# Kernel tuning notes

Measured on AMD Instinct MI355X. Metric: run time of the kernel, lower is better.

Reference implementation:

```python
import jax, jax.numpy as jnp
import numpy as np

N_EMBD = 1024
N_HEAD = 16

def setup_inputs() -> dict:
    key = jax.random.key(0)
    k1, k2, k3, k4, k5 = jax.random.split(key, 5)
    C = N_EMBD
    s = 1.0 / np.sqrt(C)
    return {
        "x": jax.random.normal(k1, (2, 2048, C), dtype=jnp.float32),
        "W_attn": jax.random.normal(k2, (C, 3 * C), dtype=jnp.float32) * s,
        "b_attn": jax.random.normal(k3, (3 * C,), dtype=jnp.float32) * 0.02,
        "W_proj": jax.random.normal(k4, (C, C), dtype=jnp.float32) * s,
        "b_proj": jax.random.normal(k5, (C,), dtype=jnp.float32) * 0.02,
    }

def reference(x, W_attn, b_attn, W_proj, b_proj):
    B, T, C = x.shape
    nh = N_HEAD
    hs = C // nh
    qkv = x @ W_attn + b_attn                      # [B, T, 3C]
    q, k, v = jnp.split(qkv, 3, axis=-1)
    # [B, T, C] -> [B, nh, T, hs]
    def to_heads(t):
        return t.reshape(B, T, nh, hs).transpose(0, 2, 1, 3)
    q, k, v = to_heads(q), to_heads(k), to_heads(v)
    scale = 1.0 / np.sqrt(hs).astype(np.float32)
    att = jnp.einsum('bhqd,bhkd->bhqk', q, k) * scale   # [B, nh, T, T]
    causal = jnp.tril(jnp.ones((T, T), dtype=bool))
    att = jnp.where(causal, att, -jnp.inf)
    att = jax.nn.softmax(att, axis=-1)
    y = jnp.einsum('bhqk,bhkd->bhqd', att, v)           # [B, nh, T, hs]
    y = y.transpose(0, 2, 1, 3).reshape(B, T, C)
    return y @ W_proj + b_proj
```

## Files before the change

### kernel.cpp

```cpp
#include <hip/hip_runtime.h>
#include <hip/hip_bf16.h>
#include <math.h>

#define N_EMBD 1024
#define N_HEAD 16
#define HS 64
#define BT 4096
#define TSEQ 2048

typedef float f32x4 __attribute__((ext_vector_type(4)));
typedef short bf16x8 __attribute__((ext_vector_type(8)));
typedef unsigned short u16;

static __device__ __forceinline__ u16 f2bf(float f) {
  union { float f; unsigned int u; } c; c.f = f;
  unsigned int r = c.u + 0x7FFFu + ((c.u >> 16) & 1u);
  return (u16)(r >> 16);
}

static __device__ __forceinline__ u16 f2bf_fast(float f) {
  union { __hip_bfloat16 h; u16 u; } cv;
  cv.h = __float2bfloat16(f);
  return cv.u;
}

__global__ __launch_bounds__(256) void cvt_bf16(const float* __restrict__ in,
                                                u16* __restrict__ out, int n4) {
  int i = blockIdx.x * 256 + threadIdx.x;
  if (i < n4) {
    float4 v = ((const float4*)in)[i];
    ushort4 o;
    o.x = f2bf(v.x); o.y = f2bf(v.y); o.z = f2bf(v.z); o.w = f2bf(v.w);
    ((ushort4*)out)[i] = o;
  }
}

__global__ __launch_bounds__(256) void transpose_cvt(const float* __restrict__ W,
                                                     u16* __restrict__ Wt,
                                                     int K, int N) {
  __shared__ u16 Ls[32][36];
  const int n0 = blockIdx.x * 32, k0 = blockIdx.y * 32;
  const int t = threadIdx.x;
  {
    int kk = t >> 3, nn4 = (t & 7) * 4;
    float4 v = *(const float4*)(W + (size_t)(k0 + kk) * N + n0 + nn4);
    Ls[kk][nn4 + 0] = f2bf(v.x); Ls[kk][nn4 + 1] = f2bf(v.y);
    Ls[kk][nn4 + 2] = f2bf(v.z); Ls[kk][nn4 + 3] = f2bf(v.w);
  }
  __syncthreads();
  {
    int nn = t >> 3, kk4 = (t & 7) * 4;
    ushort4 o;
    o.x = Ls[kk4 + 0][nn]; o.y = Ls[kk4 + 1][nn];
    o.z = Ls[kk4 + 2][nn]; o.w = Ls[kk4 + 3][nn];
    *(ushort4*)(Wt + (size_t)(n0 + nn) * K + k0 + kk4) = o;
  }
}

#define BKS 32

__device__ __forceinline__ int swz(int row, int c) {
  return row * 4 + (c ^ ((row >> 1) & 3));
}

__device__ __forceinline__ void stage128x32(const u16* __restrict__ G, int ldk,
                                            u16* lds, int w, int lane) {
#pragma unroll
  for (int i = 0; i < 2; ++i) {
    int s = i * 256 + w * 64 + lane;
    int row = s >> 2, c = s & 3;
    int csrc = c ^ ((row >> 1) & 3);
    const u16* src = G + (size_t)row * ldk + csrc * 8;
    u16* dst = lds + (size_t)(i * 256 + w * 64) * 8;
    __builtin_amdgcn_global_load_lds(
        (const __attribute__((address_space(1))) void*)src,
        (__attribute__((address_space(3))) void*)dst, 16, 0, 0);
  }
}

#define GEMM_MAIN_LOOP(Aptr, Bptr, Kdim)                                        \
  __shared__ u16 sm[2][2][128 * BKS];                                           \
  const int tid = threadIdx.x, lane = tid & 63, w = tid >> 6;                   \
  const int wr = w >> 1, wc = w & 1, lrow = lane & 15, lhi = lane >> 4;         \
  const int bm = blockIdx.y * 128, bn = blockIdx.x * 128;                       \
  f32x4 acc[4][4];                                                              \
  _Pragma("unroll") for (int i = 0; i < 4; ++i)                                 \
      _Pragma("unroll") for (int j = 0; j < 4; ++j)                             \
          acc[i][j] = (f32x4){0.f, 0.f, 0.f, 0.f};                              \
  stage128x32(Aptr + (size_t)bm * Kdim, Kdim, sm[0][0], w, lane);               \
  stage128x32(Bptr + (size_t)bn * Kdim, Kdim, sm[0][1], w, lane);               \
  __syncthreads();                                                              \
  const int NT = Kdim / BKS;                                                    \
  for (int t = 0; t < NT; ++t) {                                                \
    int cur = t & 1, nxt = cur ^ 1;                                             \
    if (t + 1 < NT) {                                                           \
      stage128x32(Aptr + (size_t)bm * Kdim + (t + 1) * BKS, Kdim, sm[nxt][0],   \
                  w, lane);                                                     \
      stage128x32(Bptr + (size_t)bn * Kdim + (t + 1) * BKS, Kdim, sm[nxt][1],   \
                  w, lane);                                                     \
    }                                                                           \
    const u16* As = sm[cur][0];                                                 \
    const u16* Bs = sm[cur][1];                                                 \
    bf16x8 af[4], bfr[4];                                                       \
    _Pragma("unroll") for (int mi = 0; mi < 4; ++mi) {                          \
      int row = wr * 64 + mi * 16 + lrow;                                       \
      af[mi] = *(const bf16x8*)(As + (size_t)swz(row, lhi) * 8);                \
    }                                                                           \
    _Pragma("unroll") for (int nj = 0; nj < 4; ++nj) {                          \
      int row = wc * 64 + nj * 16 + lrow;                                       \
      bfr[nj] = *(const bf16x8*)(Bs + (size_t)swz(row, lhi) * 8);               \
    }                                                                           \
    _Pragma("unroll") for (int mi = 0; mi < 4; ++mi)                            \
        _Pragma("unroll") for (int nj = 0; nj < 4; ++nj)                        \
            acc[mi][nj] = __builtin_amdgcn_mfma_f32_16x16x32_bf16(              \
                af[mi], bfr[nj], acc[mi][nj], 0, 0, 0);                         \
    __syncthreads();                                                            \
  }

__global__ __launch_bounds__(256) void gemm_qkv_bf16(
    const u16* __restrict__ Ab, const u16* __restrict__ Btr,
    const float* __restrict__ bias,
    u16* __restrict__ Qb, u16* __restrict__ Kb, u16* __restrict__ Vt) {
  GEMM_MAIN_LOOP(Ab, Btr, N_EMBD)
  const int sector = bn >> 10;
  const float QSC = 0.125f * 1.44269504f;
#pragma unroll
  for (int nj = 0; nj < 4; ++nj) {
    int n = bn + wc * 64 + nj * 16 + lrow;
    int h = (n & 1023) >> 6, d = n & 63;
    float bv = bias[n];
#pragma unroll
    for (int mi = 0; mi < 4; ++mi) {
      int mbase = bm + wr * 64 + mi * 16 + lhi * 4;
      int bb_ = mbase >> 11, tt = mbase & 2047;
      if (sector == 0) {
#pragma unroll
        for (int r = 0; r < 4; ++r)
          Qb[((size_t)(bb_ * 16 + h) * TSEQ + tt + r) * HS + d] =
              f2bf((acc[mi][nj][r] + bv) * QSC);
      } else if (sector == 1) {
#pragma unroll
        for (int r = 0; r < 4; ++r)
          Kb[((size_t)(bb_ * 16 + h) * TSEQ + tt + r) * HS + d] =
              f2bf(acc[mi][nj][r] + bv);
      } else {
        ushort4 o;
        o.x = f2bf(acc[mi][nj][0] + bv); o.y = f2bf(acc[mi][nj][1] + bv);
        o.z = f2bf(acc[mi][nj][2] + bv); o.w = f2bf(acc[mi][nj][3] + bv);
        *(ushort4*)(Vt + ((size_t)(bb_ * 16 + h) * HS + d) * TSEQ + tt) = o;
      }
    }
  }
}

__global__ __launch_bounds__(256) void gemm_proj_bf16(
    const u16* __restrict__ Ab, const u16* __restrict__ Btr,
    const float* __restrict__ bias, float* __restrict__ C) {
  GEMM_MAIN_LOOP(Ab, Btr, N_EMBD)
#pragma unroll
  for (int nj = 0; nj < 4; ++nj) {
    int n = bn + wc * 64 + nj * 16 + lrow;
    float bv = bias[n];
#pragma unroll
    for (int mi = 0; mi < 4; ++mi) {
      int mbase = bm + wr * 64 + mi * 16 + lhi * 4;
#pragma unroll
      for (int r = 0; r < 4; ++r)
        C[(size_t)(mbase + r) * N_EMBD + n] = acc[mi][nj][r] + bv;
    }
  }
}

__device__ __forceinline__ void stage_kv(const u16* __restrict__ Kh,
                                         const u16* __restrict__ Vh,
                                         int kb, u16* kbuf, u16* vbuf,
                                         int tid, int w) {
#pragma unroll
  for (int i = 0; i < 2; ++i) {
    int s = i * 256 + tid;
    int r = s >> 3, c = s & 7;
    int cs = c ^ (r & 7);
    const u16* ksrc = Kh + (size_t)(kb + r) * HS + cs * 8;
    u16* kdst = kbuf + (size_t)(i * 256 + (w << 6)) * 8;
    __builtin_amdgcn_global_load_lds(
        (const __attribute__((address_space(1))) void*)ksrc,
        (__attribute__((address_space(3))) void*)kdst, 16, 0, 0);
    const u16* vsrc = Vh + (size_t)r * TSEQ + kb + cs * 8;
    u16* vdst = vbuf + (size_t)(i * 256 + (w << 6)) * 8;
    __builtin_amdgcn_global_load_lds(
        (const __attribute__((address_space(1))) void*)vsrc,
        (__attribute__((address_space(3))) void*)vdst, 16, 0, 0);
  }
}

__global__ __launch_bounds__(256, 2) void attn_mfma(
    const u16* __restrict__ Qb, const u16* __restrict__ Kb,
    const u16* __restrict__ Vt, u16* __restrict__ Y) {
  __shared__ u16 Ks[2][64 * HS];
  __shared__ u16 Vs[2][64 * HS];
  __shared__ u16 Plds[4][32][72];

  const int tid  = threadIdx.x;
  const int lane = tid & 63;
  const int w    = tid >> 6;
  const int lrow = lane & 15;
  const int lhi  = lane >> 4;

  const int wg  = blockIdx.x;
  const int xcd = wg & 7;
  const int lin = wg >> 3;
  const int bhl = lin >> 4;
  const int u   = lin & 15;
  const int j   = (lin & 32) ? u : (15 - u);
  const int bh  = (xcd << 2) | bhl;
  const int b   = bh >> 4, h = bh & 15;

  const u16* Qh = Qb + (size_t)bh * TSEQ * HS;
  const u16* Kh = Kb + (size_t)bh * TSEQ * HS;
  const u16* Vh = Vt + (size_t)bh * HS * TSEQ;

  const int q0 = j * 128 + w * 32;
  const int nsteps = 2 * j + 2;

  bf16x8 aq[4];
  aq[0] = *(const bf16x8*)(Qh + (size_t)(q0 + lrow) * HS + lhi * 8);
  aq[1] = *(const bf16x8*)(Qh + (size_t)(q0 + lrow) * HS + 32 + lhi * 8);
  aq[2] = *(const bf16x8*)(Qh + (size_t)(q0 + 16 + lrow) * HS + lhi * 8);
  aq[3] = *(const bf16x8*)(Qh + (size_t)(q0 + 16 + lrow) * HS + 32 + lhi * 8);

  bf16x8 ones;
#pragma unroll
  for (int i = 0; i < 8; ++i) ones[i] = (short)0x3F80;

  f32x4 o[2][4], ol[2];
#pragma unroll
  for (int sub = 0; sub < 2; ++sub) {
    ol[sub] = (f32x4){0.f, 0.f, 0.f, 0.f};
#pragma unroll
    for (int ds = 0; ds < 4; ++ds) o[sub][ds] = (f32x4){0.f, 0.f, 0.f, 0.f};
  }

  stage_kv(Kh, Vh, 0, Ks[0], Vs[0], tid, w);

  int kb = 0;
  for (int t = 0; t < nsteps; ++t) {
    const int cur = t & 1;
    __syncthreads();
    if (t + 1 < nsteps)
      stage_kv(Kh, Vh, kb + 64, Ks[cur ^ 1], Vs[cur ^ 1], tid, w);

    const u16* Kc = Ks[cur];
    const u16* Vc = Vs[cur];

    f32x4 sacc[2][4];
#pragma unroll
    for (int s = 0; s < 4; ++s) {
      int r = s * 16 + lrow;
      bf16x8 k0 = *(const bf16x8*)(Kc + r * HS + ((lhi    ) ^ (r & 7)) * 8);
      bf16x8 k1 = *(const bf16x8*)(Kc + r * HS + ((lhi + 4) ^ (r & 7)) * 8);
      f32x4 z0 = (f32x4){0.f, 0.f, 0.f, 0.f};
      f32x4 z1 = (f32x4){0.f, 0.f, 0.f, 0.f};
      z0 = __builtin_amdgcn_mfma_f32_16x16x32_bf16(aq[0], k0, z0, 0, 0, 0);
      z0 = __builtin_amdgcn_mfma_f32_16x16x32_bf16(aq[1], k1, z0, 0, 0, 0);
      z1 = __builtin_amdgcn_mfma_f32_16x16x32_bf16(aq[2], k0, z1, 0, 0, 0);
      z1 = __builtin_amdgcn_mfma_f32_16x16x32_bf16(aq[3], k1, z1, 0, 0, 0);
      sacc[0][s] = z0; sacc[1][s] = z1;
    }

#pragma unroll
    for (int sub = 0; sub < 2; ++sub) {
      const int qbase = q0 + sub * 16;
      if (kb + 63 > qbase) {
#pragma unroll
        for (int s = 0; s < 4; ++s) {
          int kg = kb + 16 * s + lrow;
#pragma unroll
          for (int r = 0; r < 4; ++r)
            if (kg > qbase + lhi * 4 + r) sacc[sub][s][r] = -3.0e38f;
        }
      }
#pragma unroll
      for (int s = 0; s < 4; ++s)
#pragma unroll
        for (int r = 0; r < 4; ++r)
          Plds[w][sub * 16 + lhi * 4 + r][s * 16 + lrow] =
              f2bf_fast(exp2f(sacc[sub][s][r] - 16.0f));
    }

#pragma unroll
    for (int ks = 0; ks < 2; ++ks) {
      bf16x8 pa0 = *(const bf16x8*)&Plds[w][lrow][ks * 32 + lhi * 8];
      bf16x8 pa1 = *(const bf16x8*)&Plds[w][16 + lrow][ks * 32 + lhi * 8];
      ol[0] = __builtin_amdgcn_mfma_f32_16x16x32_bf16(pa0, ones, ol[0], 0, 0, 0);
      ol[1] = __builtin_amdgcn_mfma_f32_16x16x32_bf16(pa1, ones, ol[1], 0, 0, 0);
#pragma unroll
      for (int ds = 0; ds < 4; ++ds) {
        int vr = ds * 16 + lrow;
        bf16x8 vf = *(const bf16x8*)(Vc + vr * 64 + ((ks * 4 + lhi) ^ (vr & 7)) * 8);
        o[0][ds] = __builtin_amdgcn_mfma_f32_16x16x32_bf16(pa0, vf, o[0][ds], 0, 0, 0);
        o[1][ds] = __builtin_amdgcn_mfma_f32_16x16x32_bf16(pa1, vf, o[1][ds], 0, 0, 0);
      }
    }
    kb += 64;
  }

#pragma unroll
  for (int sub = 0; sub < 2; ++sub)
#pragma unroll
    for (int r = 0; r < 4; ++r) {
      float inv = 1.0f / ol[sub][r];
      int q = q0 + sub * 16 + lhi * 4 + r;
#pragma unroll
      for (int ds = 0; ds < 4; ++ds)
        Y[((size_t)(b * TSEQ + q)) * N_EMBD + h * HS + ds * 16 + lrow] =
            f2bf(o[sub][ds][r] * inv);
    }
}

extern "C" void kernel_launch(void* const* d_in, const int* in_sizes, int n_in,
                              void* d_out, int out_size, void* d_ws, size_t ws_size,
                              hipStream_t stream) {
  const float* x      = (const float*)d_in[0];
  const float* W_attn = (const float*)d_in[1];
  const float* b_attn = (const float*)d_in[2];
  const float* W_proj = (const float*)d_in[3];
  const float* b_proj = (const float*)d_in[4];
  float* out = (float*)d_out;

  u16* xb  = (u16*)d_ws;
  u16* Wat = xb  + (size_t)BT * N_EMBD;
  u16* Wpt = Wat + (size_t)3 * N_EMBD * N_EMBD;
  u16* Qb  = Wpt + (size_t)N_EMBD * N_EMBD;
  u16* Kb  = Qb  + (size_t)BT * N_EMBD;
  u16* Vt  = Kb  + (size_t)BT * N_EMBD;
  u16* yb  = Vt  + (size_t)BT * N_EMBD;

  cvt_bf16<<<(BT * N_EMBD / 4 + 255) / 256, 256, 0, stream>>>(x, xb, BT * N_EMBD / 4);
  {
    dim3 g1(3 * N_EMBD / 32, N_EMBD / 32);
    transpose_cvt<<<g1, 256, 0, stream>>>(W_attn, Wat, N_EMBD, 3 * N_EMBD);
    dim3 g2(N_EMBD / 32, N_EMBD / 32);
    transpose_cvt<<<g2, 256, 0, stream>>>(W_proj, Wpt, N_EMBD, N_EMBD);
  }
  {
    dim3 grid(3 * N_EMBD / 128, BT / 128);
    gemm_qkv_bf16<<<grid, 256, 0, stream>>>(xb, Wat, b_attn, Qb, Kb, Vt);
  }
  {
    attn_mfma<<<512, 256, 0, stream>>>(Qb, Kb, Vt, yb);
  }
  {
    dim3 grid(N_EMBD / 128, BT / 128);
    gemm_proj_bf16<<<grid, 256, 0, stream>>>(yb, Wpt, b_proj, out);
  }
}
```

Before: 135.4 us.

## Split long causal attention tiles across two workgroups with a combine pass

```diff
diff --git a/kernel.cpp b/kernel.cpp
--- a/kernel.cpp
+++ b/kernel.cpp
@@ -193,9 +193,10 @@
   }
 }
 
-__global__ __launch_bounds__(256, 2) void attn_mfma(
+__global__ __launch_bounds__(256, 2) void attn_part(
     const u16* __restrict__ Qb, const u16* __restrict__ Kb,
-    const u16* __restrict__ Vt, u16* __restrict__ Y) {
+    const u16* __restrict__ Vt, u16* __restrict__ Y,
+    float* __restrict__ Pf, float* __restrict__ Lf) {
   __shared__ u16 Ks[2][64 * HS];
   __shared__ u16 Vs[2][64 * HS];
   __shared__ u16 Plds[4][32][72];
@@ -209,18 +210,21 @@
   const int wg  = blockIdx.x;
   const int xcd = wg & 7;
   const int lin = wg >> 3;
-  const int bhl = lin >> 4;
-  const int u   = lin & 15;
-  const int j   = (lin & 32) ? u : (15 - u);
-  const int bh  = (xcd << 2) | bhl;
-  const int b   = bh >> 4, h = bh & 15;
+  const int bhl = lin / 24;
+  const int p   = lin % 24;
+  int j, half, split;
+  if (p < 16) { j = 15 - (p >> 1); half = p & 1; split = 1; }
+  else        { j = 23 - p;        half = 0;     split = 0; }
+  const int bh = (xcd << 2) | bhl;
+  const int b  = bh >> 4, h = bh & 15;
 
   const u16* Qh = Qb + (size_t)bh * TSEQ * HS;
   const u16* Kh = Kb + (size_t)bh * TSEQ * HS;
   const u16* Vh = Vt + (size_t)bh * HS * TSEQ;
 
   const int q0 = j * 128 + w * 32;
-  const int nsteps = 2 * j + 2;
+  const int nsteps = split ? (j + 1) : (2 * j + 2);
+  int kb = split ? (half * (j + 1) * 64) : 0;
 
   bf16x8 aq[4];
   aq[0] = *(const bf16x8*)(Qh + (size_t)(q0 + lrow) * HS + lhi * 8);
@@ -240,9 +244,8 @@
     for (int ds = 0; ds < 4; ++ds) o[sub][ds] = (f32x4){0.f, 0.f, 0.f, 0.f};
   }
 
-  stage_kv(Kh, Vh, 0, Ks[0], Vs[0], tid, w);
-
-  int kb = 0;
+  stage_kv(Kh, Vh, kb, Ks[0], Vs[0], tid, w);
+
   for (int t = 0; t < nsteps; ++t) {
     const int cur = t & 1;
     __syncthreads();
@@ -304,17 +307,54 @@
     kb += 64;
   }
 
-#pragma unroll
-  for (int sub = 0; sub < 2; ++sub)
-#pragma unroll
-    for (int r = 0; r < 4; ++r) {
-      float inv = 1.0f / ol[sub][r];
-      int q = q0 + sub * 16 + lhi * 4 + r;
-#pragma unroll
-      for (int ds = 0; ds < 4; ++ds)
-        Y[((size_t)(b * TSEQ + q)) * N_EMBD + h * HS + ds * 16 + lrow] =
-            f2bf(o[sub][ds][r] * inv);
-    }
+  if (!split) {
+#pragma unroll
+    for (int sub = 0; sub < 2; ++sub)
+#pragma unroll
+      for (int r = 0; r < 4; ++r) {
+        float inv = 1.0f / ol[sub][r];
+        int q = q0 + sub * 16 + lhi * 4 + r;
+#pragma unroll
+        for (int ds = 0; ds < 4; ++ds)
+          Y[((size_t)(b * TSEQ + q)) * N_EMBD + h * HS + ds * 16 + lrow] =
+              f2bf(o[sub][ds][r] * inv);
+      }
+  } else {
+    const int slot = (((bh << 3) | (j - 8)) << 1) | half;
+    float* orow = Pf + (size_t)slot * (128 * 64);
+#pragma unroll
+    for (int sub = 0; sub < 2; ++sub)
+#pragma unroll
+      for (int r = 0; r < 4; ++r) {
+        int row = w * 32 + sub * 16 + lhi * 4 + r;
+#pragma unroll
+        for (int ds = 0; ds < 4; ++ds)
+          orow[row * 64 + ds * 16 + lrow] = o[sub][ds][r];
+        if (lrow == 0) Lf[slot * 128 + row] = ol[sub][r];
+      }
+  }
+}
+
+__global__ __launch_bounds__(256) void attn_combine(
+    const float* __restrict__ Pf, const float* __restrict__ Lf,
+    u16* __restrict__ Y) {
+  const int bi = blockIdx.x;
+  const int bh = bi >> 3, jj = 8 + (bi & 7);
+  const int b  = bh >> 4, h = bh & 15;
+  const int s0 = (((bh << 3) | (jj - 8)) << 1);
+  const int tid = threadIdx.x;
+  const int d   = tid & 63;
+  const int rg  = tid >> 6;
+
+  const float* o0 = Pf + (size_t)s0 * (128 * 64);
+  const float* o1 = o0 + (128 * 64);
+  for (int rr = 0; rr < 32; ++rr) {
+    int row = rg * 32 + rr;
+    float l = Lf[s0 * 128 + row] + Lf[(s0 + 1) * 128 + row];
+    float o = o0[row * 64 + d] + o1[row * 64 + d];
+    int q = jj * 128 + row;
+    Y[((size_t)(b * TSEQ + q)) * N_EMBD + h * HS + d] = f2bf(o / l);
+  }
 }
 
 extern "C" void kernel_launch(void* const* d_in, const int* in_sizes, int n_in,
@@ -334,6 +374,8 @@
   u16* Kb  = Qb  + (size_t)BT * N_EMBD;
   u16* Vt  = Kb  + (size_t)BT * N_EMBD;
   u16* yb  = Vt  + (size_t)BT * N_EMBD;
+  float* Pf = (float*)(yb + (size_t)BT * N_EMBD);
+  float* Lf = Pf + (size_t)512 * 128 * 64;
 
   cvt_bf16<<<(BT * N_EMBD / 4 + 255) / 256, 256, 0, stream>>>(x, xb, BT * N_EMBD / 4);
   {
@@ -347,7 +389,8 @@
     gemm_qkv_bf16<<<grid, 256, 0, stream>>>(xb, Wat, b_attn, Qb, Kb, Vt);
   }
   {
-    attn_mfma<<<512, 256, 0, stream>>>(Qb, Kb, Vt, yb);
+    attn_part<<<768, 256, 0, stream>>>(Qb, Kb, Vt, yb, Pf, Lf);
+    attn_combine<<<256, 256, 0, stream>>>(Pf, Lf, yb);
   }
   {
     dim3 grid(N_EMBD / 128, BT / 128);
```

Measured after the change: 133.9 us. About the same (-1.1%).
